# Kernel optimization log

Hardware: AMD Instinct MI355X
Metric: run time of the kernel (lower is better)

The kernel has to match this reference:

```python
import jax, jax.numpy as jnp
import numpy as np

HQ, HKV = 16, 4          # query heads, kv heads
ROPE_BASE = 10000.0


def _rope(t, positions):
    # t: [B, H, S, hd]; standard rotate-half RoPE over head_dim
    hd = t.shape[-1]
    inv_freq = 1.0 / (ROPE_BASE ** (jnp.arange(0, hd, 2, dtype=jnp.float32) / hd))
    freqs = positions.astype(jnp.float32)[:, None] * inv_freq[None, :]      # [S, hd/2]
    emb = jnp.concatenate([freqs, freqs], axis=-1)                           # [S, hd]
    cos = jnp.cos(emb)[None, None, :, :].astype(t.dtype)
    sin = jnp.sin(emb)[None, None, :, :].astype(t.dtype)
    t1, t2 = t[..., : hd // 2], t[..., hd // 2 :]
    rot = jnp.concatenate([-t2, t1], axis=-1)
    return t * cos + rot * sin


def setup_inputs() -> dict:
    key = jax.random.key(0)
    k0, k1, k2, k3, k4 = jax.random.split(key, 5)
    B, S, D = 2, 2048, 2048
    hd = D // HQ
    x = jax.random.normal(k0, (B, S, D), dtype=jnp.float32)
    s = 0.02
    wq = jax.random.normal(k1, (HQ * hd, D), dtype=jnp.float32) * s
    wk = jax.random.normal(k2, (HKV * hd, D), dtype=jnp.float32) * s
    wv = jax.random.normal(k3, (HKV * hd, D), dtype=jnp.float32) * s
    wo = jax.random.normal(k4, (D, HQ * hd), dtype=jnp.float32) * s
    return {"x": x, "wq": wq, "wk": wk, "wv": wv, "wo": wo}


def reference(x, wq, wk, wv, wo):
    B, S, D = x.shape
    hd = D // HQ
    G = HQ // HKV
    positions = jnp.arange(S)

    q = (x @ wq.T).reshape(B, S, HQ, hd).transpose(0, 2, 1, 3)   # [B,Hq,S,hd]
    k = (x @ wk.T).reshape(B, S, HKV, hd).transpose(0, 2, 1, 3)  # [B,Hkv,S,hd]
    v = (x @ wv.T).reshape(B, S, HKV, hd).transpose(0, 2, 1, 3)

    q = _rope(q, positions)
    k = _rope(k, positions)

    # GQA: expand KV heads to match query heads (repeat_interleave on head dim)
    k = jnp.repeat(k, G, axis=1)
    v = jnp.repeat(v, G, axis=1)

    scores = jnp.einsum("bhqd,bhkd->bhqk", q, k) / jnp.sqrt(jnp.float32(hd))
    causal = jnp.tril(jnp.ones((S, S), dtype=bool))
    scores = jnp.where(causal[None, None], scores, -jnp.inf)
    attn = jax.nn.softmax(scores, axis=-1)

    out = jnp.einsum("bhqk,bhkd->bhqd", attn, v)                 # [B,Hq,S,hd]
    out = out.transpose(0, 2, 1, 3).reshape(B, S, HQ * hd)
    return out @ wo.T
```

## Files before the change

kernel.cpp:

```cpp
#include <hip/hip_runtime.h>

#define B_   2
#define S_   2048
#define D_   2048
#define HQ_  16
#define HKV_ 4
#define HD_  128

typedef __attribute__((ext_vector_type(4))) float f32x4;
typedef __attribute__((ext_vector_type(16))) float f32x16;
typedef __attribute__((ext_vector_type(4))) short s16x4;
typedef __attribute__((ext_vector_type(8))) short s16x8;

static __device__ __forceinline__ ushort f2bf(float f) {
  uint32_t u = __float_as_uint(f);
  u += 0x7fffu + ((u >> 16) & 1u);
  return (ushort)(u >> 16);
}

static __device__ __forceinline__ void gload16(const ushort* g, ushort* l) {
  __builtin_amdgcn_global_load_lds((const __attribute__((address_space(1))) uint32_t*)(g),
                                   (__attribute__((address_space(3))) uint32_t*)(l), 16, 0, 0);
}

__global__ void cast_kernel(const float* __restrict__ in, ushort* __restrict__ out, int n) {
  int i = (blockIdx.x * blockDim.x + threadIdx.x) * 4;
  if (i + 3 < n) {
    float4 v = *(const float4*)(in + i);
    *(ushort4*)(out + i) = make_ushort4(f2bf(v.x), f2bf(v.y), f2bf(v.z), f2bf(v.w));
  }
}

__global__ __launch_bounds__(256) void gemm_nt_bf16(const ushort* __restrict__ A,
                                                    const ushort* __restrict__ Bm,
                                                    float* __restrict__ C,
                                                    int M, int N, int K, int nbx) {
  __shared__ ushort As[128 * 64];
  __shared__ ushort Bs[128 * 64];
  const int nwg = gridDim.x;
  const int per = nwg >> 3;
  const int id = blockIdx.x;
  const int wg = (id & 7) * per + (id >> 3);
  const int bx = wg % nbx, by = wg / nbx;
  const int tid  = threadIdx.x;
  const int lane = tid & 63;
  const int wave = tid >> 6;
  const int lrow = lane & 15, lgrp = lane >> 4;
  const int wm = (wave >> 1) * 64, wn = (wave & 1) * 64;
  const int brow = by * 128, bcol = bx * 128;

  f32x4 acc[4][4];
#pragma unroll
  for (int i = 0; i < 4; ++i)
#pragma unroll
    for (int j = 0; j < 4; ++j) acc[i][j] = (f32x4){0.f, 0.f, 0.f, 0.f};

  const int r_ = tid >> 3, c16 = tid & 7;
  const ushort* Abase = A + (size_t)brow * K;
  const ushort* Bbase = Bm + (size_t)bcol * K;

  for (int k0 = 0; k0 < K; k0 += 64) {
#pragma unroll
    for (int q = 0; q < 4; ++q) {
      const int row = q * 32 + r_;
      const int sc = c16 ^ (row & 7);
      gload16(Abase + (size_t)row * K + k0 + sc * 8, &As[q * 2048 + wave * 512]);
      gload16(Bbase + (size_t)row * K + k0 + sc * 8, &Bs[q * 2048 + wave * 512]);
    }
    __syncthreads();
#pragma unroll
    for (int kc = 0; kc < 2; ++kc) {
      s16x8 aF[4], bF[4];
#pragma unroll
      for (int mt = 0; mt < 4; ++mt) {
        const int row = wm + mt * 16 + lrow;
        aF[mt] = *(const s16x8*)&As[row * 64 + ((kc * 32 + lgrp * 8) ^ ((row & 7) << 3))];
      }
#pragma unroll
      for (int nt = 0; nt < 4; ++nt) {
        const int row = wn + nt * 16 + lrow;
        bF[nt] = *(const s16x8*)&Bs[row * 64 + ((kc * 32 + lgrp * 8) ^ ((row & 7) << 3))];
      }
#pragma unroll
      for (int mt = 0; mt < 4; ++mt)
#pragma unroll
        for (int nt = 0; nt < 4; ++nt)
          acc[mt][nt] = __builtin_amdgcn_mfma_f32_16x16x32_bf16(aF[mt], bF[nt], acc[mt][nt], 0, 0, 0);
    }
    __syncthreads();
  }
#pragma unroll
  for (int mt = 0; mt < 4; ++mt) {
#pragma unroll
    for (int nt = 0; nt < 4; ++nt) {
      const int row = brow + wm + mt * 16 + lgrp * 4;
      const int col = bcol + wn + nt * 16 + lrow;
#pragma unroll
      for (int rr = 0; rr < 4; ++rr)
        C[(size_t)(row + rr) * N + col] = acc[mt][nt][rr];
    }
  }
}

__global__ void rope_qk(const float* __restrict__ qkv, ushort* __restrict__ Qb, ushort* __restrict__ Kb) {
  int idx = blockIdx.x * 256 + threadIdx.x;
  int i  = idx & 63;
  int t  = idx >> 6;
  int h2 = t % 20;
  int t2 = t / 20;
  int s  = t2 & (S_ - 1);
  int b  = t2 >> 11;
  float inv = exp2f(-(float)i * 0.20762050594046832f);
  float f = (float)s * inv;
  float sn, cs;
  sincosf(f, &sn, &cs);
  size_t row = (size_t)(b * S_ + s) * 3072;
  if (h2 < HQ_) {
    const float SCL2 = 0.12751744716705736f;
    int h = h2;
    float a = qkv[row + h * 128 + i];
    float c2 = qkv[row + h * 128 + i + 64];
    size_t ob = ((size_t)((b * HQ_ + h) * S_ + s)) * 128;
    Qb[ob + i]      = f2bf((a * cs - c2 * sn) * SCL2);
    Qb[ob + i + 64] = f2bf((c2 * cs + a * sn) * SCL2);
  } else {
    int kh = h2 - HQ_;
    float a = qkv[row + 2048 + kh * 128 + i];
    float c2 = qkv[row + 2048 + kh * 128 + i + 64];
    size_t ob = ((size_t)((b * HKV_ + kh) * S_ + s)) * 128;
    Kb[ob + i]      = f2bf(a * cs - c2 * sn);
    Kb[ob + i + 64] = f2bf(c2 * cs + a * sn);
  }
}

__global__ __launch_bounds__(256) void v_transpose(const float* __restrict__ qkv, ushort* __restrict__ Vt) {
  __shared__ ushort tile[128][72];
  const int s0 = blockIdx.x * 64;
  const int kh = blockIdx.y;
  const int b  = blockIdx.z;
  for (int idx = threadIdx.x; idx < 64 * 128; idx += 256) {
    int sl = idx >> 7;
    int d  = idx & 127;
    float v = qkv[(size_t)(b * S_ + s0 + sl) * 3072 + 2560 + kh * 128 + d];
    tile[d][sl] = f2bf(v);
  }
  __syncthreads();
  for (int idx = threadIdx.x; idx < 64 * 128; idx += 256) {
    int d  = idx >> 6;
    int sl = idx & 63;
    int sp = (sl & 48) | (sl & 3) | ((sl & 8) >> 1) | ((sl & 4) << 1);
    Vt[((size_t)(b * HKV_ + kh) * 128 + d) * S_ + s0 + sp] = tile[d][sl];
  }
}

__global__ __launch_bounds__(256, 1) void attn_kernel(const ushort* __restrict__ Qb,
                                                      const ushort* __restrict__ Kb,
                                                      const ushort* __restrict__ Vt,
                                                      ushort* __restrict__ Ao) {
  __shared__ ushort Ks[2][64 * 128];
  __shared__ ushort Vs[2][128 * 64];
  const int h = blockIdx.y, b = blockIdx.z, kh = h >> 2;
  const int tid = threadIdx.x, lane = tid & 63, wave = tid >> 6;
  const int lq = lane & 31, g = lane >> 5;
  const ushort* Kg = Kb + ((size_t)(b * HKV_ + kh)) * S_ * HD_;
  const ushort* Vg = Vt + ((size_t)(b * HKV_ + kh)) * HD_ * S_;

#pragma unroll 1
  for (int half = 0; half < 2; ++half) {
    const int qt = half ? (15 - (int)blockIdx.x) : (int)blockIdx.x;
    const int q0 = qt * 128;
    const int qg = q0 + wave * 32 + lq;
    const int nk = 2 * qt + 2;

    s16x8 qF[8];
    {
      const ushort* qrow = Qb + (((size_t)(b * HQ_ + h)) * S_ + q0 + wave * 32 + lq) * HD_ + g * 8;
#pragma unroll
      for (int s = 0; s < 8; ++s) qF[s] = *(const s16x8*)(qrow + s * 16);
    }

#define STAGE(buf, kt64)                                                          \
    {                                                                             \
      _Pragma("unroll")                                                           \
      for (int i_ = 0; i_ < 4; ++i_) {                                            \
        const int slot = i_ * 256 + tid;                                          \
        const int r = slot >> 4, c = slot & 15;                                   \
        const int cc = c ^ (r & 15);                                              \
        gload16(Kg + ((size_t)((kt64) * 64 + r)) * HD_ + cc * 8,                  \
                &Ks[buf][i_ * 2048 + wave * 512]);                                \
      }                                                                           \
      _Pragma("unroll")                                                           \
      for (int i_ = 0; i_ < 4; ++i_) {                                            \
        const int slot = i_ * 256 + tid;                                          \
        const int r = slot >> 3, c = slot & 7;                                    \
        const int cc = c ^ (r & 7);                                               \
        gload16(Vg + (size_t)r * S_ + (kt64) * 64 + cc * 8,                       \
                &Vs[buf][i_ * 2048 + wave * 512]);                                \
      }                                                                           \
    }

    STAGE(0, 0);

    f32x16 acc[4] = {};
    float m_run = -3.0e38f, l_run = 0.f;

    asm volatile("s_waitcnt vmcnt(0)" ::: "memory");
    __syncthreads();

    for (int kt = 0; kt < nk; ++kt) {
      const int cur = kt & 1;
      if (kt + 1 < nk) STAGE(cur ^ 1, kt + 1);
      const ushort* Kc = &Ks[cur][0];
      const ushort* Vc = &Vs[cur][0];

      f32x16 sacc[2];
#pragma unroll
      for (int t = 0; t < 2; ++t) {
        f32x16 a = {};
        const int row = t * 32 + lq;
#pragma unroll
        for (int s = 0; s < 8; ++s) {
          const int cc = (s * 2 + g) ^ (row & 15);
          const s16x8 kA = *(const s16x8*)(Kc + row * 128 + cc * 8);
          a = __builtin_amdgcn_mfma_f32_32x32x16_bf16(kA, qF[s], a, 0, 0, 0);
        }
        sacc[t] = a;
      }

      float tmax = -3.0e38f;
      if (kt >= 2 * qt) {
#pragma unroll
        for (int t = 0; t < 2; ++t)
#pragma unroll
          for (int r = 0; r < 16; ++r) {
            const int kg = kt * 64 + t * 32 + (r & 3) + 8 * (r >> 2) + 4 * g;
            if (kg > qg) sacc[t][r] = -3.0e38f;
            tmax = fmaxf(tmax, sacc[t][r]);
          }
      } else {
#pragma unroll
        for (int t = 0; t < 2; ++t)
#pragma unroll
          for (int r = 0; r < 16; ++r) tmax = fmaxf(tmax, sacc[t][r]);
      }
      tmax = fmaxf(tmax, __shfl_xor(tmax, 32, 64));

      if (!__all(tmax <= m_run + 8.f)) {
        const float m_new = fmaxf(m_run, tmax);
        const float alpha = exp2f(m_run - m_new);
        m_run = m_new;
        l_run *= alpha;
#pragma unroll
        for (int dt = 0; dt < 4; ++dt)
#pragma unroll
          for (int r = 0; r < 16; ++r) acc[dt][r] *= alpha;
      }

      float psum = 0.f;
      uint32_t pk[16];
#pragma unroll
      for (int t = 0; t < 2; ++t)
#pragma unroll
        for (int i = 0; i < 8; ++i) {
          const float e0 = exp2f(sacc[t][2 * i]     - m_run);
          const float e1 = exp2f(sacc[t][2 * i + 1] - m_run);
          psum += e0 + e1;
          asm("v_cvt_pk_bf16_f32 %0, %1, %2" : "=v"(pk[t * 8 + i]) : "v"(e0), "v"(e1));
        }
      psum += __shfl_xor(psum, 32, 64);
      l_run += psum;

#pragma unroll
      for (int ks = 0; ks < 4; ++ks) {
        union { s16x8 v; uint32_t u[4]; } pb;
#pragma unroll
        for (int j = 0; j < 4; ++j) pb.u[j] = pk[ks * 4 + j];
#pragma unroll
        for (int dt = 0; dt < 4; ++dt) {
          const int row = dt * 32 + lq;
          const int cc = (ks * 2 + g) ^ (row & 7);
          const s16x8 vA = *(const s16x8*)(Vc + row * 64 + cc * 8);
          acc[dt] = __builtin_amdgcn_mfma_f32_32x32x16_bf16(vA, pb.v, acc[dt], 0, 0, 0);
        }
      }

      asm volatile("s_waitcnt vmcnt(0)" ::: "memory");
      __syncthreads();
    }

    const float inv_l = 1.f / l_run;
    ushort* orow = Ao + ((size_t)(b * S_ + qg)) * D_ + h * HD_;
#pragma unroll
    for (int dt = 0; dt < 4; ++dt)
#pragma unroll
      for (int u = 0; u < 4; ++u) {
        ushort4 w;
        w.x = f2bf(acc[dt][4 * u + 0] * inv_l);
        w.y = f2bf(acc[dt][4 * u + 1] * inv_l);
        w.z = f2bf(acc[dt][4 * u + 2] * inv_l);
        w.w = f2bf(acc[dt][4 * u + 3] * inv_l);
        *(ushort4*)(orow + dt * 32 + 8 * u + 4 * g) = w;
      }
#undef STAGE
  }
}

extern "C" void kernel_launch(void* const* d_in, const int* in_sizes, int n_in,
                              void* d_out, int out_size, void* d_ws, size_t ws_size,
                              hipStream_t stream) {
  const float* x  = (const float*)d_in[0];
  const float* wq = (const float*)d_in[1];
  const float* wk = (const float*)d_in[2];
  const float* wv = (const float*)d_in[3];
  const float* wo = (const float*)d_in[4];
  float* out = (float*)d_out;
  char* ws = (char*)d_ws;

  ushort* xb    = (ushort*)(ws);
  ushort* wqkvb = (ushort*)(ws + 16777216);
  ushort* wob   = (ushort*)(ws + 29360128);
  float*  qkvf  = (float*) (ws + 37748736);
  ushort* Qb    = (ushort*)(ws + 88080384);
  ushort* Kb    = (ushort*)(ws + 104857600);
  ushort* Vt    = (ushort*)(ws + 109051904);
  ushort* Ao    = (ushort*)(ws + 113246208);

  cast_kernel<<<8192, 256, 0, stream>>>(x,  xb, 8388608);
  cast_kernel<<<4096, 256, 0, stream>>>(wq, wqkvb, 4194304);
  cast_kernel<<<1024, 256, 0, stream>>>(wk, wqkvb + 4194304, 1048576);
  cast_kernel<<<1024, 256, 0, stream>>>(wv, wqkvb + 5242880, 1048576);
  cast_kernel<<<4096, 256, 0, stream>>>(wo, wob, 4194304);

  gemm_nt_bf16<<<768, 256, 0, stream>>>(xb, wqkvb, qkvf, 4096, 3072, 2048, 24);
  rope_qk<<<20480, 256, 0, stream>>>(qkvf, Qb, Kb);
  v_transpose<<<dim3(32, 4, 2), 256, 0, stream>>>(qkvf, Vt);
  attn_kernel<<<dim3(8, 16, 2), 256, 0, stream>>>(Qb, Kb, Vt, Ao);
  gemm_nt_bf16<<<512, 256, 0, stream>>>(Ao, wob, out, 4096, 2048, 2048, 16);
}
```

Before: 347.8 us.

## Split attention q-tiles across blocks, unroll KV loop by two, amortize RoPE sincos

The attention kernel no longer loops over two paired q-tiles per block. It launches one block per q-tile (16x16x2 grid) and reverses tile order by batch for load balance, with launch bounds raised to allow two blocks per CU. The KV loop is manually unrolled by two with fixed buffer indices, precomputed swizzled LDS byte offsets, and s_setprio raised around the MFMA sections. RoPE now computes one sincos per (token, dim) and reuses it across all 16 Q and 4 K heads, cutting the grid from 20480 to 1024 blocks. Risks include the odd-nk assumption (nk is always even, so this holds), occupancy limited by LDS and registers, and less load balancing within each block.

```diff
diff --git a/kernel.cpp b/kernel.cpp
--- a/kernel.cpp
+++ b/kernel.cpp
@@ -102,32 +102,31 @@
   }
 }
 
-__global__ void rope_qk(const float* __restrict__ qkv, ushort* __restrict__ Qb, ushort* __restrict__ Kb) {
-  int idx = blockIdx.x * 256 + threadIdx.x;
-  int i  = idx & 63;
-  int t  = idx >> 6;
-  int h2 = t % 20;
-  int t2 = t / 20;
-  int s  = t2 & (S_ - 1);
-  int b  = t2 >> 11;
-  float inv = exp2f(-(float)i * 0.20762050594046832f);
-  float f = (float)s * inv;
+__global__ __launch_bounds__(256) void rope_qk(const float* __restrict__ qkv,
+                                               ushort* __restrict__ Qb, ushort* __restrict__ Kb) {
+  const int idx = blockIdx.x * 256 + threadIdx.x;
+  const int i = idx & 63;
+  const int t = idx >> 6;
+  const int s = t & (S_ - 1);
+  const int b = t >> 11;
+  const float inv = exp2f(-(float)i * 0.20762050594046832f);
   float sn, cs;
-  sincosf(f, &sn, &cs);
-  size_t row = (size_t)(b * S_ + s) * 3072;
-  if (h2 < HQ_) {
-    const float SCL2 = 0.12751744716705736f;
-    int h = h2;
-    float a = qkv[row + h * 128 + i];
-    float c2 = qkv[row + h * 128 + i + 64];
-    size_t ob = ((size_t)((b * HQ_ + h) * S_ + s)) * 128;
+  sincosf((float)s * inv, &sn, &cs);
+  const size_t row = (size_t)t * 3072;
+  const float SCL2 = 0.12751744716705736f;
+#pragma unroll
+  for (int h = 0; h < HQ_; ++h) {
+    const float a  = qkv[row + h * 128 + i];
+    const float c2 = qkv[row + h * 128 + i + 64];
+    const size_t ob = ((size_t)((b * HQ_ + h) * S_ + s)) * 128;
     Qb[ob + i]      = f2bf((a * cs - c2 * sn) * SCL2);
     Qb[ob + i + 64] = f2bf((c2 * cs + a * sn) * SCL2);
-  } else {
-    int kh = h2 - HQ_;
-    float a = qkv[row + 2048 + kh * 128 + i];
-    float c2 = qkv[row + 2048 + kh * 128 + i + 64];
-    size_t ob = ((size_t)((b * HKV_ + kh) * S_ + s)) * 128;
+  }
+#pragma unroll
+  for (int kh = 0; kh < HKV_; ++kh) {
+    const float a  = qkv[row + 2048 + kh * 128 + i];
+    const float c2 = qkv[row + 2048 + kh * 128 + i + 64];
+    const size_t ob = ((size_t)((b * HKV_ + kh) * S_ + s)) * 128;
     Kb[ob + i]      = f2bf(a * cs - c2 * sn);
     Kb[ob + i + 64] = f2bf(c2 * cs + a * sn);
   }
@@ -153,7 +152,7 @@
   }
 }
 
-__global__ __launch_bounds__(256, 1) void attn_kernel(const ushort* __restrict__ Qb,
+__global__ __launch_bounds__(256, 2) void attn_kernel(const ushort* __restrict__ Qb,
                                                       const ushort* __restrict__ Kb,
                                                       const ushort* __restrict__ Vt,
                                                       ushort* __restrict__ Ao) {
@@ -165,19 +164,25 @@
   const ushort* Kg = Kb + ((size_t)(b * HKV_ + kh)) * S_ * HD_;
   const ushort* Vg = Vt + ((size_t)(b * HKV_ + kh)) * HD_ * S_;
 
-#pragma unroll 1
-  for (int half = 0; half < 2; ++half) {
-    const int qt = half ? (15 - (int)blockIdx.x) : (int)blockIdx.x;
-    const int q0 = qt * 128;
-    const int qg = q0 + wave * 32 + lq;
-    const int nk = 2 * qt + 2;
-
-    s16x8 qF[8];
-    {
-      const ushort* qrow = Qb + (((size_t)(b * HQ_ + h)) * S_ + q0 + wave * 32 + lq) * HD_ + g * 8;
-#pragma unroll
-      for (int s = 0; s < 8; ++s) qF[s] = *(const s16x8*)(qrow + s * 16);
-    }
+  const int qt = b ? (15 - (int)blockIdx.x) : (int)blockIdx.x;
+  const int q0 = qt * 128;
+  const int qg = q0 + wave * 32 + lq;
+  const int nk = 2 * qt + 2;
+
+  s16x8 qF[8];
+  {
+    const ushort* qrow = Qb + (((size_t)(b * HQ_ + h)) * S_ + qg) * HD_ + g * 8;
+#pragma unroll
+    for (int s = 0; s < 8; ++s) qF[s] = *(const s16x8*)(qrow + s * 16);
+  }
+
+  const char* KsB = (const char*)&Ks[0][0];
+  const char* VsB = (const char*)&Vs[0][0];
+  uint32_t ka[2], va[4];
+#pragma unroll
+  for (int t = 0; t < 2; ++t) ka[t] = (uint32_t)(t * 32 + lq) * 256 + ((uint32_t)(g ^ (lq & 15)) << 4);
+#pragma unroll
+  for (int dt = 0; dt < 4; ++dt) va[dt] = (uint32_t)(dt * 32 + lq) * 128 + ((uint32_t)(g ^ (lq & 7)) << 4);
 
 #define STAGE(buf, kt64)                                                          \
     {                                                                             \
@@ -199,110 +204,107 @@
       }                                                                           \
     }
 
-    STAGE(0, 0);
-
-    f32x16 acc[4] = {};
-    float m_run = -3.0e38f, l_run = 0.f;
-
+  f32x16 acc[4] = {};
+  float m_run = -3.0e38f, l_run = 0.f;
+
+  STAGE(0, 0);
+  asm volatile("s_waitcnt vmcnt(0)" ::: "memory");
+  __syncthreads();
+
+#define COMPUTE(CUR, ktv)                                                                   \
+  {                                                                                         \
+    f32x16 sc[2] = {};                                                                      \
+    __builtin_amdgcn_s_setprio(1);                                                          \
+    _Pragma("unroll")                                                                       \
+    for (int s = 0; s < 8; ++s) {                                                           \
+      const s16x8 k0 = *(const s16x8*)(KsB + (ka[0] ^ (uint32_t)(s << 5)) + (CUR)*16384);   \
+      const s16x8 k1 = *(const s16x8*)(KsB + (ka[1] ^ (uint32_t)(s << 5)) + (CUR)*16384);   \
+      sc[0] = __builtin_amdgcn_mfma_f32_32x32x16_bf16(k0, qF[s], sc[0], 0, 0, 0);           \
+      sc[1] = __builtin_amdgcn_mfma_f32_32x32x16_bf16(k1, qF[s], sc[1], 0, 0, 0);           \
+    }                                                                                       \
+    __builtin_amdgcn_s_setprio(0);                                                          \
+    float tmax = -3.0e38f;                                                                  \
+    if ((ktv) >= 2 * qt) {                                                                  \
+      _Pragma("unroll")                                                                     \
+      for (int t = 0; t < 2; ++t)                                                           \
+        _Pragma("unroll")                                                                   \
+        for (int r = 0; r < 16; ++r) {                                                      \
+          const int kg = (ktv) * 64 + t * 32 + (r & 3) + 8 * (r >> 2) + 4 * g;              \
+          if (kg > qg) sc[t][r] = -3.0e38f;                                                 \
+          tmax = fmaxf(tmax, sc[t][r]);                                                     \
+        }                                                                                   \
+    } else {                                                                                \
+      _Pragma("unroll")                                                                     \
+      for (int t = 0; t < 2; ++t)                                                           \
+        _Pragma("unroll")                                                                   \
+        for (int r = 0; r < 16; ++r) tmax = fmaxf(tmax, sc[t][r]);                          \
+    }                                                                                       \
+    tmax = fmaxf(tmax, __shfl_xor(tmax, 32, 64));                                           \
+    if (!__all(tmax <= m_run + 8.f)) {                                                      \
+      const float m_new = fmaxf(m_run, tmax);                                               \
+      const float alpha = exp2f(m_run - m_new);                                             \
+      m_run = m_new;                                                                        \
+      l_run *= alpha;                                                                       \
+      _Pragma("unroll")                                                                     \
+      for (int dt = 0; dt < 4; ++dt)                                                        \
+        _Pragma("unroll")                                                                   \
+        for (int r = 0; r < 16; ++r) acc[dt][r] *= alpha;                                   \
+    }                                                                                       \
+    float psum = 0.f;                                                                       \
+    uint32_t pk[16];                                                                        \
+    _Pragma("unroll")                                                                       \
+    for (int t = 0; t < 2; ++t)                                                             \
+      _Pragma("unroll")                                                                     \
+      for (int i = 0; i < 8; ++i) {                                                         \
+        const float e0 = exp2f(sc[t][2 * i]     - m_run);                                   \
+        const float e1 = exp2f(sc[t][2 * i + 1] - m_run);                                   \
+        psum += e0 + e1;                                                                    \
+        asm("v_cvt_pk_bf16_f32 %0, %1, %2" : "=v"(pk[t * 8 + i]) : "v"(e0), "v"(e1));       \
+      }                                                                                     \
+    psum += __shfl_xor(psum, 32, 64);                                                       \
+    l_run += psum;                                                                          \
+    __builtin_amdgcn_s_setprio(1);                                                          \
+    _Pragma("unroll")                                                                       \
+    for (int ks = 0; ks < 4; ++ks) {                                                        \
+      union { s16x8 v; uint32_t u[4]; } pb;                                                 \
+      _Pragma("unroll")                                                                     \
+      for (int j = 0; j < 4; ++j) pb.u[j] = pk[ks * 4 + j];                                 \
+      _Pragma("unroll")                                                                     \
+      for (int dt = 0; dt < 4; ++dt) {                                                      \
+        const s16x8 vA = *(const s16x8*)(VsB + (va[dt] ^ (uint32_t)(ks << 5)) + (CUR)*16384);\
+        acc[dt] = __builtin_amdgcn_mfma_f32_32x32x16_bf16(vA, pb.v, acc[dt], 0, 0, 0);      \
+      }                                                                                     \
+    }                                                                                       \
+    __builtin_amdgcn_s_setprio(0);                                                          \
+  }
+
+#pragma unroll 1
+  for (int kt = 0; kt < nk; kt += 2) {
+    STAGE(1, kt + 1);
+    COMPUTE(0, kt);
     asm volatile("s_waitcnt vmcnt(0)" ::: "memory");
     __syncthreads();
-
-    for (int kt = 0; kt < nk; ++kt) {
-      const int cur = kt & 1;
-      if (kt + 1 < nk) STAGE(cur ^ 1, kt + 1);
-      const ushort* Kc = &Ks[cur][0];
-      const ushort* Vc = &Vs[cur][0];
-
-      f32x16 sacc[2];
-#pragma unroll
-      for (int t = 0; t < 2; ++t) {
-        f32x16 a = {};
-        const int row = t * 32 + lq;
-#pragma unroll
-        for (int s = 0; s < 8; ++s) {
-          const int cc = (s * 2 + g) ^ (row & 15);
-          const s16x8 kA = *(const s16x8*)(Kc + row * 128 + cc * 8);
-          a = __builtin_amdgcn_mfma_f32_32x32x16_bf16(kA, qF[s], a, 0, 0, 0);
-        }
-        sacc[t] = a;
-      }
-
-      float tmax = -3.0e38f;
-      if (kt >= 2 * qt) {
-#pragma unroll
-        for (int t = 0; t < 2; ++t)
-#pragma unroll
-          for (int r = 0; r < 16; ++r) {
-            const int kg = kt * 64 + t * 32 + (r & 3) + 8 * (r >> 2) + 4 * g;
-            if (kg > qg) sacc[t][r] = -3.0e38f;
-            tmax = fmaxf(tmax, sacc[t][r]);
-          }
-      } else {
-#pragma unroll
-        for (int t = 0; t < 2; ++t)
-#pragma unroll
-          for (int r = 0; r < 16; ++r) tmax = fmaxf(tmax, sacc[t][r]);
-      }
-      tmax = fmaxf(tmax, __shfl_xor(tmax, 32, 64));
-
-      if (!__all(tmax <= m_run + 8.f)) {
-        const float m_new = fmaxf(m_run, tmax);
-        const float alpha = exp2f(m_run - m_new);
-        m_run = m_new;
-        l_run *= alpha;
-#pragma unroll
-        for (int dt = 0; dt < 4; ++dt)
-#pragma unroll
-          for (int r = 0; r < 16; ++r) acc[dt][r] *= alpha;
-      }
-
-      float psum = 0.f;
-      uint32_t pk[16];
-#pragma unroll
-      for (int t = 0; t < 2; ++t)
-#pragma unroll
-        for (int i = 0; i < 8; ++i) {
-          const float e0 = exp2f(sacc[t][2 * i]     - m_run);
-          const float e1 = exp2f(sacc[t][2 * i + 1] - m_run);
-          psum += e0 + e1;
-          asm("v_cvt_pk_bf16_f32 %0, %1, %2" : "=v"(pk[t * 8 + i]) : "v"(e0), "v"(e1));
-        }
-      psum += __shfl_xor(psum, 32, 64);
-      l_run += psum;
-
-#pragma unroll
-      for (int ks = 0; ks < 4; ++ks) {
-        union { s16x8 v; uint32_t u[4]; } pb;
-#pragma unroll
-        for (int j = 0; j < 4; ++j) pb.u[j] = pk[ks * 4 + j];
-#pragma unroll
-        for (int dt = 0; dt < 4; ++dt) {
-          const int row = dt * 32 + lq;
-          const int cc = (ks * 2 + g) ^ (row & 7);
-          const s16x8 vA = *(const s16x8*)(Vc + row * 64 + cc * 8);
-          acc[dt] = __builtin_amdgcn_mfma_f32_32x32x16_bf16(vA, pb.v, acc[dt], 0, 0, 0);
-        }
-      }
-
-      asm volatile("s_waitcnt vmcnt(0)" ::: "memory");
-      __syncthreads();
-    }
-
-    const float inv_l = 1.f / l_run;
-    ushort* orow = Ao + ((size_t)(b * S_ + qg)) * D_ + h * HD_;
-#pragma unroll
-    for (int dt = 0; dt < 4; ++dt)
-#pragma unroll
-      for (int u = 0; u < 4; ++u) {
-        ushort4 w;
-        w.x = f2bf(acc[dt][4 * u + 0] * inv_l);
-        w.y = f2bf(acc[dt][4 * u + 1] * inv_l);
-        w.z = f2bf(acc[dt][4 * u + 2] * inv_l);
-        w.w = f2bf(acc[dt][4 * u + 3] * inv_l);
-        *(ushort4*)(orow + dt * 32 + 8 * u + 4 * g) = w;
-      }
+    if (kt + 2 < nk) STAGE(0, kt + 2);
+    COMPUTE(1, kt + 1);
+    asm volatile("s_waitcnt vmcnt(0)" ::: "memory");
+    __syncthreads();
+  }
+
+  const float inv_l = 1.f / l_run;
+  ushort* orow = Ao + ((size_t)(b * S_ + qg)) * D_ + h * HD_;
+#pragma unroll
+  for (int dt = 0; dt < 4; ++dt)
+#pragma unroll
+    for (int u = 0; u < 4; ++u) {
+      ushort4 w;
+      w.x = f2bf(acc[dt][4 * u + 0] * inv_l);
+      w.y = f2bf(acc[dt][4 * u + 1] * inv_l);
+      w.z = f2bf(acc[dt][4 * u + 2] * inv_l);
+      w.w = f2bf(acc[dt][4 * u + 3] * inv_l);
+      *(ushort4*)(orow + dt * 32 + 8 * u + 4 * g) = w;
+    }
 #undef STAGE
-  }
+#undef COMPUTE
 }
 
 extern "C" void kernel_launch(void* const* d_in, const int* in_sizes, int n_in,
@@ -332,8 +334,8 @@
   cast_kernel<<<4096, 256, 0, stream>>>(wo, wob, 4194304);
 
   gemm_nt_bf16<<<768, 256, 0, stream>>>(xb, wqkvb, qkvf, 4096, 3072, 2048, 24);
-  rope_qk<<<20480, 256, 0, stream>>>(qkvf, Qb, Kb);
+  rope_qk<<<1024, 256, 0, stream>>>(qkvf, Qb, Kb);
   v_transpose<<<dim3(32, 4, 2), 256, 0, stream>>>(qkvf, Vt);
-  attn_kernel<<<dim3(8, 16, 2), 256, 0, stream>>>(Qb, Kb, Vt, Ao);
+  attn_kernel<<<dim3(16, 16, 2), 256, 0, stream>>>(Qb, Kb, Vt, Ao);
   gemm_nt_bf16<<<512, 256, 0, stream>>>(Ao, wob, out, 4096, 2048, 2048, 16);
 }
```

After: 333.0 us. -4.3%, faster.
